# Performance work log

Measured on AMD Instinct MI355X. Metric: run time of the kernel, lower is better.

## Reference

```python
import jax, jax.numpy as jnp
import numpy as np

N_T = 200
THR = 0.6
ALPHA = 0.8   # hard-coded in __init__
KAPPA = 0.8   # hard-coded in __init__
RHO = 0.97
BETA = 0.07
SCALE = 50.0  # get_pos scale
# norse defaults used by ConstantCurrentLIFEncoder / LILinearCell
DT = 1e-3
TAU_MEM_INV = 100.0
TAU_SYN_INV = 200.0
V_TH = 1.0


def encode_constant_current(I):
    """norse ConstantCurrentLIFEncoder: LIF driven by constant current I [n_b, f] -> spikes [n_t, n_b, f]."""
    def step(v, _):
        v = v + DT * TAU_MEM_INV * (I - v)          # dv = dt*tau_mem_inv*((v_leak - v) + I), v_leak=0
        z = (v > V_TH).astype(I.dtype)
        v = v * (1.0 - z)                            # reset to v_reset=0 on spike
        return v, z
    _, zs = jax.lax.scan(step, jnp.zeros_like(I), None, length=N_T)
    return zs


def setup_inputs() -> dict:
    key = jax.random.key(0)
    ks = jax.random.split(key, 5)
    n_b, n_feat = 128, 512
    n_in, n_rec, n_out = 2 * n_feat, 2048, 32
    x = jax.random.normal(ks[0], (n_b, n_feat), jnp.float32)
    # kaiming_normal_ std = sqrt(2/fan_in), then scaled by w_init_gain
    w_in = jax.random.normal(ks[1], (n_rec, n_in), jnp.float32) * (0.5 * np.sqrt(2.0 / n_in))
    w_rec = jax.random.normal(ks[2], (n_rec, n_rec), jnp.float32) * (0.1 * np.sqrt(2.0 / n_rec))
    w_out = jax.random.normal(ks[3], (n_out, n_rec), jnp.float32) * (0.5 * np.sqrt(2.0 / n_rec))
    w_li = jax.random.normal(ks[4], (1, n_rec), jnp.float32) * np.sqrt(2.0 / n_rec)
    return {"x": x, "w_in": w_in, "w_rec": w_rec, "w_out": w_out, "w_li": w_li}


def reference(x, w_in, w_rec, w_out, w_li):
    n_rec = w_rec.shape[0]
    n_out = w_out.shape[0]
    n_b = x.shape[0]
    # get_pos: pos/neg rectified constant-current LIF encoding, cat on feature dim -> [n_t, n_b, n_in]
    xs = jnp.concatenate([
        encode_constant_current(jax.nn.relu(SCALE * x)),
        encode_constant_current(jax.nn.relu(-SCALE * x)),
    ], axis=2)
    # zero self-recurrence: w_rec *= (1 - I)
    w_rec = w_rec * (1.0 - jnp.eye(n_rec, dtype=w_rec.dtype))

    def step(carry, x_t):
        v, a, z, vo, li_v, li_i = carry
        # ALIF membrane update + adaptive threshold spike
        v = ALPHA * v + z @ w_rec.T + x_t @ w_in.T - z * THR
        a = RHO * a + z
        z = (v > THR + BETA * a).astype(v.dtype)
        # (dropout p=0.5 treated as identity / eval mode)
        vo = KAPPA * vo + z @ w_out.T
        # norse LILinearCell critic readout (li_step)
        i_jump = li_i + z @ w_li.T
        li_v = li_v + DT * TAU_MEM_INV * (i_jump - li_v)
        li_i = i_jump - DT * TAU_SYN_INV * i_jump
        return (v, a, z, vo, li_v, li_i), (vo, li_v)

    zeros = lambda d: jnp.zeros((n_b, d), x.dtype)
    carry0 = (zeros(n_rec), zeros(n_rec), zeros(n_rec), zeros(n_out), zeros(1), zeros(1))
    _, (vo_seq, vc_seq) = jax.lax.scan(step, carry0, xs[: N_T - 1])  # loop runs n_t-1 steps
    # torch.max over time includes the all-zero t=0 row -> clamp max with 0
    m = jnp.maximum(jnp.max(vo_seq, axis=0), 0.0)          # [n_b, n_out]
    yo = jax.nn.softmax(m, axis=1)
    critic_value = jnp.maximum(jnp.max(vc_seq, axis=0), 0.0)  # [n_b, 1]
    return yo, critic_value
```

## Files before the change

### kernel.cpp

```cpp
#include <hip/hip_runtime.h>
#include <cstdint>
#include <cstddef>

typedef __attribute__((ext_vector_type(8))) short short8;
typedef __attribute__((ext_vector_type(4))) float f32x4;
typedef __attribute__((ext_vector_type(4))) unsigned int u32x4;

union U4S8 { u32x4 u; short8 s; unsigned w[4]; };

#define TSTEPS 199

#define WF_PLANE 786432u
#define WR_BASE  1572864u
#define WR_PLANE 12288u

#define WS_BAR  0u
#define WS_ZB   4096u
#define WS_FIN  135168u
#define WS_XSB  151552u
#define WS_WF   3411968u
#define WS_NEED 28971008u

#define AT_RLX __ATOMIC_RELAXED
#define SC_AGT __HIP_MEMORY_SCOPE_AGENT

extern "C" __global__ __launch_bounds__(1024) void k_encode(
    const float* __restrict__ x, unsigned char* __restrict__ xsb)
{
  const int b = blockIdx.x;
  const int tid = threadIdx.x;
  const float xv = (tid < 512) ? x[b * 512 + tid] : x[b * 512 + tid - 512];
  const float I = (tid < 512) ? fmaxf(__fmul_rn(50.0f, xv), 0.0f)
                              : fmaxf(__fmul_rn(-50.0f, xv), 0.0f);
  float v = 0.0f;
  unsigned long long* dst =
      (unsigned long long*)(xsb + (size_t)b * 128u + (size_t)(tid >> 6) * 8u);
  for (int t = 0; t < TSTEPS; ++t) {
    v = __fadd_rn(v, __fmul_rn(0.1f, __fsub_rn(I, v)));
    const bool z = v > 1.0f;
    if (z) v = 0.0f;
    const unsigned long long m = __ballot(z ? 1 : 0);
    if ((tid & 63) == 0) dst[(size_t)t * 2048u] = m;
  }
}

__device__ __forceinline__ unsigned bf16rne(float f) {
  const unsigned u = __float_as_uint(f);
  return ((u + 0x7FFFu + ((u >> 16) & 1u)) >> 16) & 0xFFFFu;
}

extern "C" __global__ __launch_bounds__(256) void k_prep(
    const float* __restrict__ w_rec, const float* __restrict__ w_in,
    const float* __restrict__ w_out, const float* __restrict__ w_li,
    u32x4* __restrict__ wf)
{
  const unsigned idx  = blockIdx.x * 256u + threadIdx.x;
  const unsigned lane = idx & 63u;
  if (idx < 786432u) {
    const unsigned kt = (idx >> 6) % 96u;
    const unsigned ns = idx / 6144u;
    const unsigned j  = ns * 16u + (lane & 15u);
    const unsigned k0 = kt * 32u + (lane >> 4) * 8u;
    unsigned hi[4], lo[4];
#pragma unroll
    for (int u2 = 0; u2 < 4; ++u2) {
      unsigned hb[2], lb[2];
#pragma unroll
      for (int c = 0; c < 2; ++c) {
        const unsigned k = k0 + 2u * (unsigned)u2 + (unsigned)c;
        float w;
        if (k < 2048u) w = (k == j) ? 0.0f : w_rec[(size_t)j * 2048u + k];
        else           w = w_in[(size_t)j * 1024u + (k - 2048u)];
        const unsigned h = bf16rne(w);
        const float hvf = __uint_as_float(h << 16);
        const unsigned l = bf16rne(__fsub_rn(w, hvf));
        hb[c] = h; lb[c] = l;
      }
      hi[u2] = hb[0] | (hb[1] << 16);
      lo[u2] = lb[0] | (lb[1] << 16);
    }
    u32x4 vh, vl;
    vh[0]=hi[0]; vh[1]=hi[1]; vh[2]=hi[2]; vh[3]=hi[3];
    vl[0]=lo[0]; vl[1]=lo[1]; vl[2]=lo[2]; vl[3]=lo[3];
    wf[idx] = vh;
    wf[idx + WF_PLANE] = vl;
  } else if (idx < 786432u + 12288u) {
    const unsigned r   = idx - 786432u;
    const unsigned kt  = (r >> 6) & 63u;
    const unsigned nsr = r >> 12;
    const unsigned o   = nsr * 16u + (lane & 15u);
    const unsigned k0  = kt * 32u + (lane >> 4) * 8u;
    unsigned hi[4], lo[4];
#pragma unroll
    for (int u2 = 0; u2 < 4; ++u2) {
      unsigned hb[2], lb[2];
#pragma unroll
      for (int c = 0; c < 2; ++c) {
        const unsigned k = k0 + 2u * (unsigned)u2 + (unsigned)c;
        float w = 0.0f;
        if (o < 32u)       w = w_out[(size_t)o * 2048u + k];
        else if (o == 32u) w = w_li[k];
        const unsigned h = bf16rne(w);
        const float hvf = __uint_as_float(h << 16);
        hb[c] = h;
        lb[c] = bf16rne(__fsub_rn(w, hvf));
      }
      hi[u2] = hb[0] | (hb[1] << 16);
      lo[u2] = lb[0] | (lb[1] << 16);
    }
    u32x4 vh, vl;
    vh[0]=hi[0]; vh[1]=hi[1]; vh[2]=hi[2]; vh[3]=hi[3];
    vl[0]=lo[0]; vl[1]=lo[1]; vl[2]=lo[2]; vl[3]=lo[3];
    wf[WR_BASE + r] = vh;
    wf[WR_BASE + WR_PLANE + r] = vl;
  }
}

__device__ __forceinline__ void bar_arrive(unsigned* dbar, unsigned ns)
{
  __syncthreads();
  if (threadIdx.x == 0) {
    __hip_atomic_fetch_add(dbar + (ns >> 4) * 16u, 1u, AT_RLX, SC_AGT);
  }
}

__device__ __forceinline__ void bar_wait16(unsigned* dbar, unsigned tgt16)
{
  if (threadIdx.x == 0) {
    for (;;) {
      unsigned mn = 0xFFFFFFFFu;
#pragma unroll
      for (int g = 0; g < 8; ++g) {
        const unsigned c = __hip_atomic_load(dbar + g * 16, AT_RLX, SC_AGT);
        mn = (c < mn) ? c : mn;
      }
      if (mn >= tgt16) break;
      __builtin_amdgcn_s_sleep(1);
    }
    asm volatile("" ::: "memory");
  }
  __syncthreads();
}

extern "C" __global__ __launch_bounds__(512, 2) void k_main(
    const u32x4* __restrict__ wf,
    const unsigned char* __restrict__ xsb,
    unsigned* __restrict__ zb,
    unsigned* __restrict__ bar,
    unsigned* __restrict__ fin,
    float* __restrict__ out)
{
  __shared__ unsigned abytes[64][100];
  __shared__ float red[8][64][17];
  __shared__ unsigned char zn[64][4];
  __shared__ float pad_lds[6000];

  const unsigned tid  = threadIdx.x;
  const unsigned wg   = blockIdx.x;
  const unsigned mh   = wg >> 7;
  const unsigned ns   = wg & 127u;
  const unsigned wv   = tid >> 6;
  const unsigned lane = tid & 63u;
  const unsigned ln15 = lane & 15u;
  const unsigned g4   = lane >> 4;
  const unsigned selr = g4 * 0x01010101u;
  const unsigned blq  = tid & 63u;
  const unsigned q    = tid >> 6;
  const bool     upd  = tid < 256u;
  const bool     dual = ns < 3u;

  if (tid == 0) ((volatile float*)pad_lds)[0] = 0.f;

  unsigned* dbar = bar + mh * 256u;

  const u32x4* WH = wf + (size_t)ns * 6144u;
  const u32x4* WL = wf + WF_PLANE + (size_t)ns * 6144u;
  const u32x4* RH = wf + WR_BASE + (size_t)ns * 4096u;

  float v[4]  = {0,0,0,0}, a[4] = {0,0,0,0}, zf[4] = {0,0,0,0};
  float vo[4] = {0,0,0,0}, voMax[4] = {0,0,0,0};
  float liv = 0.f, lii = 0.f, liMax = 0.f;

  f32x4 accX0 = {0,0,0,0}, accX1 = {0,0,0,0}, accX2 = {0,0,0,0}, accX3 = {0,0,0,0};
  U4S8 bhZ[8], blZ[8];
  U4S8 bhX[4], blX[4];
  const int zk = (int)wv * 8;
  const int xk = 64 + (int)wv * 4;

  auto pk = [](unsigned long long t) -> unsigned {
    return (unsigned)(t & 0xFFFFu) | (unsigned)(((t >> 32) & 0xFFFFu) << 16);
  };

  auto stage_xs = [&](int t) {
    const unsigned char* xr = xsb + ((size_t)t * 128u + mh * 64u) * 128u;
    const u32x4 val = *(const u32x4*)(xr + (size_t)lane * 128u + wv * 16u);
    *(u32x4*)&abytes[lane][64u + wv * 4u] = val;
  };

  auto mk = [&](unsigned dw, U4S8& af) {
    const unsigned sp = __builtin_amdgcn_perm(dw, dw, selr);
    const unsigned W  = ((sp >> 1) & 0xFFFF0000u) | (sp & 0x0000FFFFu);
    af.w[0] = __umul24(W & 0x00010001u, 0x3F80u);
    af.w[1] = __umul24(W & 0x00040004u, 0x0FE0u);
    af.w[2] = __umul24(W & 0x00100010u, 0x03F8u);
    af.w[3] = __umul24(W & 0x00400040u, 0x00FEu);
  };

  auto dosub2 = [&](unsigned dw, const short8& bhj, const short8& blj, f32x4& ACC) {
    U4S8 af; mk(dw, af);
    ACC = __builtin_amdgcn_mfma_f32_16x16x32_bf16(af.s, bhj, ACC, 0, 0, 0);
    ACC = __builtin_amdgcn_mfma_f32_16x16x32_bf16(af.s, blj, ACC, 0, 0, 0);
  };

  auto grp4 = [&](int kb, const U4S8* bh, const U4S8* bl) {
    U4S8 a0, a1, a2, a3;
    a0.u = *(const u32x4*)&abytes[ 0 + ln15][kb];
    a1.u = *(const u32x4*)&abytes[16 + ln15][kb];
    a2.u = *(const u32x4*)&abytes[32 + ln15][kb];
    a3.u = *(const u32x4*)&abytes[48 + ln15][kb];
#pragma unroll
    for (int j = 0; j < 4; ++j) {
      dosub2(a0.w[j], bh[j].s, bl[j].s, accX0);
      dosub2(a1.w[j], bh[j].s, bl[j].s, accX1);
      dosub2(a2.w[j], bh[j].s, bl[j].s, accX2);
      dosub2(a3.w[j], bh[j].s, bl[j].s, accX3);
    }
  };

  auto compute_accX = [&]() {
    accX0 = {0,0,0,0}; accX1 = {0,0,0,0}; accX2 = {0,0,0,0}; accX3 = {0,0,0,0};
    grp4(xk, bhX, blX);
  };

  auto stage_and_zpart = [&](unsigned buf) {
    const unsigned long long* zp = (const unsigned long long*)zb +
        ((size_t)((buf * 2u + mh) * 64u + lane) * 64u) + (unsigned)zk;
    unsigned long long z0 = __hip_atomic_load(zp + 0, AT_RLX, SC_AGT);
    unsigned long long z1 = __hip_atomic_load(zp + 1, AT_RLX, SC_AGT);
    unsigned long long z2 = __hip_atomic_load(zp + 2, AT_RLX, SC_AGT);
    unsigned long long z3 = __hip_atomic_load(zp + 3, AT_RLX, SC_AGT);
    unsigned long long z4 = __hip_atomic_load(zp + 4, AT_RLX, SC_AGT);
    unsigned long long z5 = __hip_atomic_load(zp + 5, AT_RLX, SC_AGT);
    unsigned long long z6 = __hip_atomic_load(zp + 6, AT_RLX, SC_AGT);
    unsigned long long z7 = __hip_atomic_load(zp + 7, AT_RLX, SC_AGT);
    u32x4 wa; wa[0] = pk(z0); wa[1] = pk(z1); wa[2] = pk(z2); wa[3] = pk(z3);
    *(u32x4*)&abytes[lane][(unsigned)zk] = wa;
    grp4(zk, &bhZ[0], &blZ[0]);
    u32x4 wb; wb[0] = pk(z4); wb[1] = pk(z5); wb[2] = pk(z6); wb[3] = pk(z7);
    *(u32x4*)&abytes[lane][(unsigned)zk + 4u] = wb;
    grp4(zk + 4, &bhZ[4], &blZ[4]);
  };

  auto redstore = [&]() {
#pragma unroll
    for (int r = 0; r < 4; ++r) {
      red[wv][ 0 + g4 * 4 + r][ln15] = accX0[r];
      red[wv][16 + g4 * 4 + r][ln15] = accX1[r];
      red[wv][32 + g4 * 4 + r][ln15] = accX2[r];
      red[wv][48 + g4 * 4 + r][ln15] = accX3[r];
    }
  };

  auto readout_pass = [&]() {
    f32x4 r0 = {0,0,0,0}, r1 = {0,0,0,0}, r2 = {0,0,0,0}, r3 = {0,0,0,0};
    const int kb = (int)wv * 8;
#pragma unroll
    for (int kc = 0; kc < 8; kc += 4) {
      U4S8 ar0, ar1, ar2, ar3;
      ar0.u = *(const u32x4*)&abytes[ 0 + ln15][kb + kc];
      ar1.u = *(const u32x4*)&abytes[16 + ln15][kb + kc];
      ar2.u = *(const u32x4*)&abytes[32 + ln15][kb + kc];
      ar3.u = *(const u32x4*)&abytes[48 + ln15][kb + kc];
      U4S8 bh[4];
#pragma unroll
      for (int j = 0; j < 4; ++j) {
        bh[j].u = RH[(size_t)(kb + kc + j) * 64u + lane];
      }
#pragma unroll
      for (int j = 0; j < 4; ++j) {
        U4S8 af0; mk(ar0.w[j], af0);
        r0 = __builtin_amdgcn_mfma_f32_16x16x32_bf16(af0.s, bh[j].s, r0, 0, 0, 0);
        U4S8 af1; mk(ar1.w[j], af1);
        r1 = __builtin_amdgcn_mfma_f32_16x16x32_bf16(af1.s, bh[j].s, r1, 0, 0, 0);
        U4S8 af2; mk(ar2.w[j], af2);
        r2 = __builtin_amdgcn_mfma_f32_16x16x32_bf16(af2.s, bh[j].s, r2, 0, 0, 0);
        U4S8 af3; mk(ar3.w[j], af3);
        r3 = __builtin_amdgcn_mfma_f32_16x16x32_bf16(af3.s, bh[j].s, r3, 0, 0, 0);
      }
    }
#pragma unroll
    for (int r = 0; r < 4; ++r) {
      red[wv][ 0 + g4 * 4 + r][ln15] = r0[r];
      red[wv][16 + g4 * 4 + r][ln15] = r1[r];
      red[wv][32 + g4 * 4 + r][ln15] = r2[r];
      red[wv][48 + g4 * 4 + r][ln15] = r3[r];
    }
    __syncthreads();
    if (upd) {
      if (ns < 2u) {
#pragma unroll
        for (int jj = 0; jj < 4; ++jj) {
          const unsigned n = q * 4u + (unsigned)jj;
          float s = ((red[0][blq][n] + red[1][blq][n]) + (red[2][blq][n] + red[3][blq][n]))
                  + ((red[4][blq][n] + red[5][blq][n]) + (red[6][blq][n] + red[7][blq][n]));
          vo[jj] = __fadd_rn(__fmul_rn(0.8f, vo[jj]), s);
          voMax[jj] = fmaxf(voMax[jj], vo[jj]);
        }
      } else if (q == 0u) {
        float s = ((red[0][blq][0] + red[1][blq][0]) + (red[2][blq][0] + red[3][blq][0]))
                + ((red[4][blq][0] + red[5][blq][0]) + (red[6][blq][0] + red[7][blq][0]));
        const float ij = __fadd_rn(lii, s);
        liv = __fadd_rn(liv, __fmul_rn(0.1f, __fsub_rn(ij, liv)));
        lii = __fsub_rn(ij, __fmul_rn(0.2f, ij));
        liMax = fmaxf(liMax, liv);
      }
    }
    __syncthreads();
  };

#pragma unroll
  for (int j = 0; j < 8; ++j) {
    bhZ[j].u = WH[(size_t)(zk + j) * 64u + lane];
    blZ[j].u = WL[(size_t)(zk + j) * 64u + lane];
  }
#pragma unroll
  for (int j = 0; j < 4; ++j) {
    bhX[j].u = WH[(size_t)(xk + j) * 64u + lane];
    blX[j].u = WL[(size_t)(xk + j) * 64u + lane];
  }
  stage_xs(0);
  compute_accX();

  for (int t = 0; t < TSTEPS; ++t) {
    if (t > 0) bar_wait16(dbar, 16u * (unsigned)t);

    stage_and_zpart((unsigned)t & 1u);
    redstore();
    __syncthreads();

    if (upd) {
      unsigned nib = 0u;
#pragma unroll
      for (int jj = 0; jj < 4; ++jj) {
        const unsigned n = q * 4u + (unsigned)jj;
        const float dv = ((red[0][blq][n] + red[1][blq][n]) + (red[2][blq][n] + red[3][blq][n]))
                       + ((red[4][blq][n] + red[5][blq][n]) + (red[6][blq][n] + red[7][blq][n]));
        const float vv = __fsub_rn(__fadd_rn(__fmul_rn(0.8f, v[jj]), dv),
                                   __fmul_rn(zf[jj], 0.6f));
        a[jj] = __fadd_rn(__fmul_rn(0.97f, a[jj]), zf[jj]);
        const float th = __fadd_rn(0.6f, __fmul_rn(0.07f, a[jj]));
        const bool znew = vv > th;
        zf[jj] = znew ? 1.0f : 0.0f;
        v[jj] = vv;
        nib |= (znew ? 1u : 0u) << jj;
      }
      zn[blq][q] = (unsigned char)nib;
    }
    __syncthreads();

    if (tid < 64u) {
      const unsigned m16 = (unsigned)zn[tid][0] | ((unsigned)zn[tid][1] << 4) |
                           ((unsigned)zn[tid][2] << 8) | ((unsigned)zn[tid][3] << 12);
      const unsigned nb = ((unsigned)t & 1u) ^ 1u;
      __hip_atomic_store(zb + ((nb * 2u + mh) * 64u + tid) * 128u + ns, m16,
                         AT_RLX, SC_AGT);
    }
    bar_arrive(dbar, ns);

    if (t < TSTEPS - 1) stage_xs(t + 1);
    if (dual && t > 0) readout_pass();
    if (t < TSTEPS - 1) compute_accX();
  }

  bar_wait16(dbar, 16u * (unsigned)TSTEPS);
  if (dual) {
    const unsigned buf = (unsigned)TSTEPS & 1u;
    const unsigned long long* zp = (const unsigned long long*)zb +
        ((size_t)((buf * 2u + mh) * 64u + lane) * 64u) + (unsigned)zk;
    u32x4 wa, wb;
    wa[0] = pk(__hip_atomic_load(zp + 0, AT_RLX, SC_AGT));
    wa[1] = pk(__hip_atomic_load(zp + 1, AT_RLX, SC_AGT));
    wa[2] = pk(__hip_atomic_load(zp + 2, AT_RLX, SC_AGT));
    wa[3] = pk(__hip_atomic_load(zp + 3, AT_RLX, SC_AGT));
    wb[0] = pk(__hip_atomic_load(zp + 4, AT_RLX, SC_AGT));
    wb[1] = pk(__hip_atomic_load(zp + 5, AT_RLX, SC_AGT));
    wb[2] = pk(__hip_atomic_load(zp + 6, AT_RLX, SC_AGT));
    wb[3] = pk(__hip_atomic_load(zp + 7, AT_RLX, SC_AGT));
    *(u32x4*)&abytes[lane][(unsigned)zk] = wa;
    *(u32x4*)&abytes[lane][(unsigned)zk + 4u] = wb;
    readout_pass();
    if (ns < 2u && upd) {
#pragma unroll
      for (int jj = 0; jj < 4; ++jj) {
        __hip_atomic_store(fin + ((size_t)mh * 64u + blq) * 32u + ns * 16u + q * 4u + (unsigned)jj,
                           __float_as_uint(voMax[jj]), AT_RLX, SC_AGT);
      }
    }
    if (ns == 2u && tid < 64u) {
      out[4096u + mh * 64u + tid] = liMax;
    }
  }
  bar_arrive(dbar, ns);

  if (ns == 0u) {
    bar_wait16(dbar, 16u * ((unsigned)TSTEPS + 1u));
    if (tid < 64u) {
      const unsigned grow = mh * 64u + tid;
      float vals[32];
#pragma unroll
      for (int o = 0; o < 32; ++o)
        vals[o] = __uint_as_float(__hip_atomic_load(fin + (size_t)grow * 32u + o,
                                                    AT_RLX, SC_AGT));
      float mx = vals[0];
#pragma unroll
      for (int o = 1; o < 32; ++o) mx = fmaxf(mx, vals[o]);
      float ssum = 0.f;
#pragma unroll
      for (int o = 0; o < 32; ++o) ssum += expf(vals[o] - mx);
      const float inv = 1.0f / ssum;
#pragma unroll
      for (int o = 0; o < 32; ++o) out[(size_t)grow * 32u + o] = expf(vals[o] - mx) * inv;
    }
  }
}

extern "C" void kernel_launch(void* const* d_in, const int* in_sizes, int n_in,
                              void* d_out, int out_size, void* d_ws, size_t ws_size,
                              hipStream_t stream)
{
  (void)in_sizes; (void)n_in; (void)out_size;
  if (ws_size < (size_t)WS_NEED) return;

  const float* x     = (const float*)d_in[0];
  const float* w_in  = (const float*)d_in[1];
  const float* w_rec = (const float*)d_in[2];
  const float* w_out = (const float*)d_in[3];
  const float* w_li  = (const float*)d_in[4];
  unsigned char* ws  = (unsigned char*)d_ws;

  unsigned*      bar  = (unsigned*)(ws + WS_BAR);
  unsigned*      zb   = (unsigned*)(ws + WS_ZB);
  unsigned*      fin  = (unsigned*)(ws + WS_FIN);
  unsigned char* xsb  = ws + WS_XSB;
  u32x4*         wf   = (u32x4*)(ws + WS_WF);

  hipMemsetAsync(ws, 0, 4096u + 131072u, stream);
  k_encode<<<dim3(128), dim3(1024), 0, stream>>>(x, xsb);
  k_prep<<<dim3(3120), dim3(256), 0, stream>>>(w_rec, w_in, w_out, w_li, wf);
  k_main<<<dim3(256), dim3(512), 0, stream>>>(wf, xsb, zb, bar, fin, (float*)d_out);
}
```

Measured before the change: 1.585 ms.

## Split batch into four 32-row domains across 512 workgroups

After: 2.397 ms. 1.51x slower.

```diff
diff --git a/kernel.cpp b/kernel.cpp
--- a/kernel.cpp
+++ b/kernel.cpp
@@ -142,7 +142,7 @@
   __syncthreads();
 }
 
-extern "C" __global__ __launch_bounds__(512, 2) void k_main(
+extern "C" __global__ __launch_bounds__(512, 4) void k_main(
     const u32x4* __restrict__ wf,
     const unsigned char* __restrict__ xsb,
     unsigned* __restrict__ zb,
@@ -150,38 +150,37 @@
     unsigned* __restrict__ fin,
     float* __restrict__ out)
 {
-  __shared__ unsigned abytes[64][100];
-  __shared__ float red[8][64][17];
-  __shared__ unsigned char zn[64][4];
+  __shared__ unsigned abytes[32][100];
+  __shared__ float red[8][32][17];
+  __shared__ unsigned char zn[32][16];
   __shared__ float pad_lds[6000];
 
   const unsigned tid  = threadIdx.x;
   const unsigned wg   = blockIdx.x;
-  const unsigned mh   = wg >> 7;
+  const unsigned dom  = wg >> 7;
   const unsigned ns   = wg & 127u;
   const unsigned wv   = tid >> 6;
   const unsigned lane = tid & 63u;
   const unsigned ln15 = lane & 15u;
   const unsigned g4   = lane >> 4;
   const unsigned selr = g4 * 0x01010101u;
-  const unsigned blq  = tid & 63u;
-  const unsigned q    = tid >> 6;
-  const bool     upd  = tid < 256u;
+  const unsigned row_u = tid & 31u;
+  const unsigned nq    = tid >> 5;
   const bool     dual = ns < 3u;
 
   if (tid == 0) ((volatile float*)pad_lds)[0] = 0.f;
 
-  unsigned* dbar = bar + mh * 256u;
+  unsigned* dbar = bar + dom * 256u;
 
   const u32x4* WH = wf + (size_t)ns * 6144u;
   const u32x4* WL = wf + WF_PLANE + (size_t)ns * 6144u;
   const u32x4* RH = wf + WR_BASE + (size_t)ns * 4096u;
 
-  float v[4]  = {0,0,0,0}, a[4] = {0,0,0,0}, zf[4] = {0,0,0,0};
-  float vo[4] = {0,0,0,0}, voMax[4] = {0,0,0,0};
+  float v = 0.f, a = 0.f, zf = 0.f;
+  float vo = 0.f, voMax = 0.f;
   float liv = 0.f, lii = 0.f, liMax = 0.f;
 
-  f32x4 accX0 = {0,0,0,0}, accX1 = {0,0,0,0}, accX2 = {0,0,0,0}, accX3 = {0,0,0,0};
+  f32x4 accX0 = {0,0,0,0}, accX1 = {0,0,0,0};
   U4S8 bhZ[8], blZ[8];
   U4S8 bhX[4], blX[4];
   const int zk = (int)wv * 8;
@@ -192,9 +191,11 @@
   };
 
   auto stage_xs = [&](int t) {
-    const unsigned char* xr = xsb + ((size_t)t * 128u + mh * 64u) * 128u;
-    const u32x4 val = *(const u32x4*)(xr + (size_t)lane * 128u + wv * 16u);
-    *(u32x4*)&abytes[lane][64u + wv * 4u] = val;
+    if (lane < 32u) {
+      const unsigned char* xr = xsb + ((size_t)t * 128u + dom * 32u) * 128u;
+      const u32x4 val = *(const u32x4*)(xr + (size_t)lane * 128u + wv * 16u);
+      *(u32x4*)&abytes[lane][64u + wv * 4u] = val;
+    }
   };
 
   auto mk = [&](unsigned dw, U4S8& af) {
@@ -213,41 +214,33 @@
   };
 
   auto grp4 = [&](int kb, const U4S8* bh, const U4S8* bl) {
-    U4S8 a0, a1, a2, a3;
+    U4S8 a0, a1;
     a0.u = *(const u32x4*)&abytes[ 0 + ln15][kb];
     a1.u = *(const u32x4*)&abytes[16 + ln15][kb];
-    a2.u = *(const u32x4*)&abytes[32 + ln15][kb];
-    a3.u = *(const u32x4*)&abytes[48 + ln15][kb];
 #pragma unroll
     for (int j = 0; j < 4; ++j) {
       dosub2(a0.w[j], bh[j].s, bl[j].s, accX0);
       dosub2(a1.w[j], bh[j].s, bl[j].s, accX1);
-      dosub2(a2.w[j], bh[j].s, bl[j].s, accX2);
-      dosub2(a3.w[j], bh[j].s, bl[j].s, accX3);
     }
   };
 
   auto compute_accX = [&]() {
-    accX0 = {0,0,0,0}; accX1 = {0,0,0,0}; accX2 = {0,0,0,0}; accX3 = {0,0,0,0};
+    accX0 = {0,0,0,0}; accX1 = {0,0,0,0};
     grp4(xk, bhX, blX);
   };
 
   auto stage_and_zpart = [&](unsigned buf) {
+    const unsigned row = lane & 31u;
+    const unsigned g2  = (lane >> 5) * 4u;
     const unsigned long long* zp = (const unsigned long long*)zb +
-        ((size_t)((buf * 2u + mh) * 64u + lane) * 64u) + (unsigned)zk;
+        ((size_t)((buf * 4u + dom) * 32u + row) * 64u) + (unsigned)zk + g2;
     unsigned long long z0 = __hip_atomic_load(zp + 0, AT_RLX, SC_AGT);
     unsigned long long z1 = __hip_atomic_load(zp + 1, AT_RLX, SC_AGT);
     unsigned long long z2 = __hip_atomic_load(zp + 2, AT_RLX, SC_AGT);
     unsigned long long z3 = __hip_atomic_load(zp + 3, AT_RLX, SC_AGT);
-    unsigned long long z4 = __hip_atomic_load(zp + 4, AT_RLX, SC_AGT);
-    unsigned long long z5 = __hip_atomic_load(zp + 5, AT_RLX, SC_AGT);
-    unsigned long long z6 = __hip_atomic_load(zp + 6, AT_RLX, SC_AGT);
-    unsigned long long z7 = __hip_atomic_load(zp + 7, AT_RLX, SC_AGT);
     u32x4 wa; wa[0] = pk(z0); wa[1] = pk(z1); wa[2] = pk(z2); wa[3] = pk(z3);
-    *(u32x4*)&abytes[lane][(unsigned)zk] = wa;
-    grp4(zk, &bhZ[0], &blZ[0]);
-    u32x4 wb; wb[0] = pk(z4); wb[1] = pk(z5); wb[2] = pk(z6); wb[3] = pk(z7);
-    *(u32x4*)&abytes[lane][(unsigned)zk + 4u] = wb;
+    *(u32x4*)&abytes[row][(unsigned)zk + g2] = wa;
+    grp4(zk,     &bhZ[0], &blZ[0]);
     grp4(zk + 4, &bhZ[4], &blZ[4]);
   };
 
@@ -256,21 +249,17 @@
     for (int r = 0; r < 4; ++r) {
       red[wv][ 0 + g4 * 4 + r][ln15] = accX0[r];
       red[wv][16 + g4 * 4 + r][ln15] = accX1[r];
-      red[wv][32 + g4 * 4 + r][ln15] = accX2[r];
-      red[wv][48 + g4 * 4 + r][ln15] = accX3[r];
     }
   };
 
   auto readout_pass = [&]() {
-    f32x4 r0 = {0,0,0,0}, r1 = {0,0,0,0}, r2 = {0,0,0,0}, r3 = {0,0,0,0};
+    f32x4 r0 = {0,0,0,0}, r1 = {0,0,0,0};
     const int kb = (int)wv * 8;
 #pragma unroll
     for (int kc = 0; kc < 8; kc += 4) {
-      U4S8 ar0, ar1, ar2, ar3;
+      U4S8 ar0, ar1;
       ar0.u = *(const u32x4*)&abytes[ 0 + ln15][kb + kc];
       ar1.u = *(const u32x4*)&abytes[16 + ln15][kb + kc];
-      ar2.u = *(const u32x4*)&abytes[32 + ln15][kb + kc];
-      ar3.u = *(const u32x4*)&abytes[48 + ln15][kb + kc];
       U4S8 bh[4];
 #pragma unroll
       for (int j = 0; j < 4; ++j) {
@@ -282,38 +271,26 @@
         r0 = __builtin_amdgcn_mfma_f32_16x16x32_bf16(af0.s, bh[j].s, r0, 0, 0, 0);
         U4S8 af1; mk(ar1.w[j], af1);
         r1 = __builtin_amdgcn_mfma_f32_16x16x32_bf16(af1.s, bh[j].s, r1, 0, 0, 0);
-        U4S8 af2; mk(ar2.w[j], af2);
-        r2 = __builtin_amdgcn_mfma_f32_16x16x32_bf16(af2.s, bh[j].s, r2, 0, 0, 0);
-        U4S8 af3; mk(ar3.w[j], af3);
-        r3 = __builtin_amdgcn_mfma_f32_16x16x32_bf16(af3.s, bh[j].s, r3, 0, 0, 0);
       }
     }
 #pragma unroll
     for (int r = 0; r < 4; ++r) {
       red[wv][ 0 + g4 * 4 + r][ln15] = r0[r];
       red[wv][16 + g4 * 4 + r][ln15] = r1[r];
-      red[wv][32 + g4 * 4 + r][ln15] = r2[r];
-      red[wv][48 + g4 * 4 + r][ln15] = r3[r];
     }
     __syncthreads();
-    if (upd) {
-      if (ns < 2u) {
-#pragma unroll
-        for (int jj = 0; jj < 4; ++jj) {
-          const unsigned n = q * 4u + (unsigned)jj;
-          float s = ((red[0][blq][n] + red[1][blq][n]) + (red[2][blq][n] + red[3][blq][n]))
-                  + ((red[4][blq][n] + red[5][blq][n]) + (red[6][blq][n] + red[7][blq][n]));
-          vo[jj] = __fadd_rn(__fmul_rn(0.8f, vo[jj]), s);
-          voMax[jj] = fmaxf(voMax[jj], vo[jj]);
-        }
-      } else if (q == 0u) {
-        float s = ((red[0][blq][0] + red[1][blq][0]) + (red[2][blq][0] + red[3][blq][0]))
-                + ((red[4][blq][0] + red[5][blq][0]) + (red[6][blq][0] + red[7][blq][0]));
-        const float ij = __fadd_rn(lii, s);
-        liv = __fadd_rn(liv, __fmul_rn(0.1f, __fsub_rn(ij, liv)));
-        lii = __fsub_rn(ij, __fmul_rn(0.2f, ij));
-        liMax = fmaxf(liMax, liv);
-      }
+    if (ns < 2u) {
+      const float s = ((red[0][row_u][nq] + red[1][row_u][nq]) + (red[2][row_u][nq] + red[3][row_u][nq]))
+                    + ((red[4][row_u][nq] + red[5][row_u][nq]) + (red[6][row_u][nq] + red[7][row_u][nq]));
+      vo = __fadd_rn(__fmul_rn(0.8f, vo), s);
+      voMax = fmaxf(voMax, vo);
+    } else if (tid < 32u) {
+      const float s = ((red[0][tid][0] + red[1][tid][0]) + (red[2][tid][0] + red[3][tid][0]))
+                    + ((red[4][tid][0] + red[5][tid][0]) + (red[6][tid][0] + red[7][tid][0]));
+      const float ij = __fadd_rn(lii, s);
+      liv = __fadd_rn(liv, __fmul_rn(0.1f, __fsub_rn(ij, liv)));
+      lii = __fsub_rn(ij, __fmul_rn(0.2f, ij));
+      liMax = fmaxf(liMax, liv);
     }
     __syncthreads();
   };
@@ -338,31 +315,30 @@
     redstore();
     __syncthreads();
 
-    if (upd) {
-      unsigned nib = 0u;
-#pragma unroll
-      for (int jj = 0; jj < 4; ++jj) {
-        const unsigned n = q * 4u + (unsigned)jj;
-        const float dv = ((red[0][blq][n] + red[1][blq][n]) + (red[2][blq][n] + red[3][blq][n]))
-                       + ((red[4][blq][n] + red[5][blq][n]) + (red[6][blq][n] + red[7][blq][n]));
-        const float vv = __fsub_rn(__fadd_rn(__fmul_rn(0.8f, v[jj]), dv),
-                                   __fmul_rn(zf[jj], 0.6f));
-        a[jj] = __fadd_rn(__fmul_rn(0.97f, a[jj]), zf[jj]);
-        const float th = __fadd_rn(0.6f, __fmul_rn(0.07f, a[jj]));
-        const bool znew = vv > th;
-        zf[jj] = znew ? 1.0f : 0.0f;
-        v[jj] = vv;
-        nib |= (znew ? 1u : 0u) << jj;
-      }
-      zn[blq][q] = (unsigned char)nib;
+    {
+      const float dv = ((red[0][row_u][nq] + red[1][row_u][nq]) + (red[2][row_u][nq] + red[3][row_u][nq]))
+                     + ((red[4][row_u][nq] + red[5][row_u][nq]) + (red[6][row_u][nq] + red[7][row_u][nq]));
+      const float vv = __fsub_rn(__fadd_rn(__fmul_rn(0.8f, v), dv),
+                                 __fmul_rn(zf, 0.6f));
+      a = __fadd_rn(__fmul_rn(0.97f, a), zf);
+      const float th = __fadd_rn(0.6f, __fmul_rn(0.07f, a));
+      const bool znew = vv > th;
+      zf = znew ? 1.0f : 0.0f;
+      v = vv;
+      zn[row_u][nq] = znew ? 1u : 0u;
     }
     __syncthreads();
 
-    if (tid < 64u) {
-      const unsigned m16 = (unsigned)zn[tid][0] | ((unsigned)zn[tid][1] << 4) |
-                           ((unsigned)zn[tid][2] << 8) | ((unsigned)zn[tid][3] << 12);
+    if (tid < 32u) {
+      const unsigned* zr = (const unsigned*)&zn[tid][0];
+      unsigned m16 = 0u;
+#pragma unroll
+      for (int b = 0; b < 4; ++b) {
+        const unsigned nib = ((zr[b] & 0x01010101u) * 0x10204080u) >> 28;
+        m16 |= nib << (4 * b);
+      }
       const unsigned nb = ((unsigned)t & 1u) ^ 1u;
-      __hip_atomic_store(zb + ((nb * 2u + mh) * 64u + tid) * 128u + ns, m16,
+      __hip_atomic_store(zb + ((nb * 4u + dom) * 32u + tid) * 128u + ns, m16,
                          AT_RLX, SC_AGT);
     }
     bar_arrive(dbar, ns);
@@ -375,37 +351,32 @@
   bar_wait16(dbar, 16u * (unsigned)TSTEPS);
   if (dual) {
     const unsigned buf = (unsigned)TSTEPS & 1u;
+    const unsigned row = lane & 31u;
+    const unsigned g2  = (lane >> 5) * 4u;
     const unsigned long long* zp = (const unsigned long long*)zb +
-        ((size_t)((buf * 2u + mh) * 64u + lane) * 64u) + (unsigned)zk;
-    u32x4 wa, wb;
+        ((size_t)((buf * 4u + dom) * 32u + row) * 64u) + (unsigned)zk + g2;
+    u32x4 wa;
     wa[0] = pk(__hip_atomic_load(zp + 0, AT_RLX, SC_AGT));
     wa[1] = pk(__hip_atomic_load(zp + 1, AT_RLX, SC_AGT));
     wa[2] = pk(__hip_atomic_load(zp + 2, AT_RLX, SC_AGT));
     wa[3] = pk(__hip_atomic_load(zp + 3, AT_RLX, SC_AGT));
-    wb[0] = pk(__hip_atomic_load(zp + 4, AT_RLX, SC_AGT));
-    wb[1] = pk(__hip_atomic_load(zp + 5, AT_RLX, SC_AGT));
-    wb[2] = pk(__hip_atomic_load(zp + 6, AT_RLX, SC_AGT));
-    wb[3] = pk(__hip_atomic_load(zp + 7, AT_RLX, SC_AGT));
-    *(u32x4*)&abytes[lane][(unsigned)zk] = wa;
-    *(u32x4*)&abytes[lane][(unsigned)zk + 4u] = wb;
+    *(u32x4*)&abytes[row][(unsigned)zk + g2] = wa;
+    __syncthreads();
     readout_pass();
-    if (ns < 2u && upd) {
-#pragma unroll
-      for (int jj = 0; jj < 4; ++jj) {
-        __hip_atomic_store(fin + ((size_t)mh * 64u + blq) * 32u + ns * 16u + q * 4u + (unsigned)jj,
-                           __float_as_uint(voMax[jj]), AT_RLX, SC_AGT);
-      }
-    }
-    if (ns == 2u && tid < 64u) {
-      out[4096u + mh * 64u + tid] = liMax;
+    if (ns < 2u) {
+      __hip_atomic_store(fin + ((size_t)dom * 32u + row_u) * 32u + ns * 16u + nq,
+                         __float_as_uint(voMax), AT_RLX, SC_AGT);
+    }
+    if (ns == 2u && tid < 32u) {
+      out[4096u + dom * 32u + tid] = liMax;
     }
   }
   bar_arrive(dbar, ns);
 
   if (ns == 0u) {
     bar_wait16(dbar, 16u * ((unsigned)TSTEPS + 1u));
-    if (tid < 64u) {
-      const unsigned grow = mh * 64u + tid;
+    if (tid < 32u) {
+      const unsigned grow = dom * 32u + tid;
       float vals[32];
 #pragma unroll
       for (int o = 0; o < 32; ++o)
@@ -447,5 +418,5 @@
   hipMemsetAsync(ws, 0, 4096u + 131072u, stream);
   k_encode<<<dim3(128), dim3(1024), 0, stream>>>(x, xsb);
   k_prep<<<dim3(3120), dim3(256), 0, stream>>>(w_rec, w_in, w_out, w_li, wf);
-  k_main<<<dim3(256), dim3(512), 0, stream>>>(wf, xsb, zb, bar, fin, (float*)d_out);
-}
+  k_main<<<dim3(512), dim3(512), 0, stream>>>(wf, xsb, zb, bar, fin, (float*)d_out);
+}
```
